# Kernel tuning notes

Hardware: AMD Instinct MI355X
Metric: run time of the kernel (lower is better)

## Reference

```python
import jax, jax.numpy as jnp
import numpy as np

N = 100000       # nodes
E = 1600000      # edges (avg degree 16)
D = 128          # features_dim = hidden_dim = out_dim
G = 3            # group_num
NUM = 50000      # nodes present in all time groups
ALPHA = 0.2      # LeakyReLU slope
W_SCALE = 0.05


def setup_inputs() -> dict:
    key = jax.random.key(0)
    ks = jax.random.split(key, 8)
    x = jax.random.normal(ks[0], (N, D), jnp.float32)
    edge_index = jax.random.randint(ks[1], (2, E), 0, N, dtype=jnp.int64)
    past = jax.random.normal(ks[2], (G - 1, NUM, D), jnp.float32)
    W1 = jax.random.normal(ks[3], (2 * D, D), jnp.float32) * W_SCALE
    W2 = jax.random.normal(ks[4], (2 * D, D), jnp.float32) * W_SCALE
    W0 = jax.random.normal(ks[5], (D, D), jnp.float32) * W_SCALE
    Wp = jax.random.normal(ks[6], (G - 1, D, D), jnp.float32) * W_SCALE
    W_T = jax.random.normal(ks[7], (2 * D, D), jnp.float32) * W_SCALE
    return {"x": x, "past": past, "W1": W1, "W2": W2, "W0": W0,
            "Wp": Wp, "W_T": W_T, "edge_index": edge_index, "num": NUM}


def reference(x, past, W1, W2, W0, Wp, W_T, edge_index, num):
    src, dst = edge_index[0], edge_index[1]
    n = x.shape[0]
    deg = jax.ops.segment_sum(jnp.ones(src.shape[0], x.dtype), dst, num_segments=n)
    deg = jnp.maximum(deg, 1.0)[:, None]

    def sage_layer(h, W):
        # mean-aggregate neighbors, concat with self, linear + ReLU
        agg = jax.ops.segment_sum(h[src], dst, num_segments=n) / deg
        return jax.nn.relu(jnp.concatenate([h, agg], axis=1) @ W)

    feat = sage_layer(x, W1)      # [N, D]
    feat = sage_layer(feat, W2)   # [N, D]

    # temporal mean aggregation (dropout is identity in eval mode)
    time_feat = (feat[:num] @ W0 + jnp.einsum('knd,kde->ne', past, Wp)) / G
    fused = jnp.concatenate([feat[:num], time_feat], axis=1) @ W_T  # [num, D]
    f = jax.nn.leaky_relu(fused, ALPHA)
    f = f / jnp.maximum(jnp.linalg.norm(f, axis=1, keepdims=True), 1e-12)
    return jnp.concatenate([f, feat[num:]], axis=0)  # [N, D]
```

## Files before the change

### kernel.cpp

```cpp
#include <hip/hip_runtime.h>

#define FD 128
#define CAP 64
#define BSH 9
#define BINSZ 512
#define NBMAX 256

typedef __attribute__((ext_vector_type(8))) short bf16x8;
typedef __attribute__((ext_vector_type(4))) float f32x4;

__device__ __forceinline__ float bflo(unsigned v) { return __uint_as_float(v << 16); }
__device__ __forceinline__ float bfhi(unsigned v) { return __uint_as_float(v & 0xffff0000u); }
__device__ __forceinline__ unsigned short f2b(float f) {
  unsigned u = __float_as_uint(f);
  return (unsigned short)((u + 0x7fffu + ((u >> 16) & 1u)) >> 16);
}
__device__ __forceinline__ unsigned pack2(float x, float y) {
  return (unsigned)f2b(x) | ((unsigned)f2b(y) << 16);
}

#if __has_builtin(__builtin_amdgcn_fdot2_f32_bf16)
#define HAVE_DOT2 1
typedef __attribute__((ext_vector_type(2))) __bf16 bf16x2;
__device__ __forceinline__ float dot2acc(unsigned v, unsigned w, float acc) {
  return __builtin_amdgcn_fdot2_f32_bf16(__builtin_bit_cast(bf16x2, v),
                                         __builtin_bit_cast(bf16x2, w), acc, false);
}
#endif

__device__ __forceinline__ void wpack_tile(const float* __restrict__ W,
                                           unsigned short* __restrict__ Wf,
                                           int nkt, int tt, int lane) {
  int ct = tt & 7, kt = tt >> 3;
  int m = lane & 15, q = lane >> 4;
  int nn = ct * 16 + m;
  int k0 = kt * 32 + q * 8;
  unsigned short tmp[8];
#pragma unroll
  for (int j = 0; j < 8; ++j) tmp[j] = f2b(W[(size_t)(k0 + j) * FD + nn]);
  unsigned short* dst = Wf + ((size_t)(ct * nkt + kt) * 64 + lane) * 8;
  *(uint4*)dst = *(uint4*)tmp;
}

__global__ __launch_bounds__(256) void k_prep(const float4* __restrict__ x4,
                                              unsigned short* __restrict__ xb, int total4,
                                              const int* __restrict__ dst,
                                              int* __restrict__ binCnt, int E, int n, int NB,
                                              const float* __restrict__ W1,
                                              const float* __restrict__ W2,
                                              const float* __restrict__ W0,
                                              const float* __restrict__ Wp,
                                              const float* __restrict__ WT,
                                              unsigned short* __restrict__ w1f,
                                              unsigned short* __restrict__ w2f,
                                              unsigned short* __restrict__ wcf,
                                              unsigned short* __restrict__ wtf,
                                              unsigned short* __restrict__ f1b,
                                              int XCB, int HB) {
  __shared__ int lh[NBMAX];
  int b = blockIdx.x, tid = threadIdx.x;

  if (b < XCB) {
    int i = b * 256 + tid;
    if (i < total4) {
      float4 v = x4[i];
      *(uint2*)&xb[(size_t)i * 4] = make_uint2(pack2(v.x, v.y), pack2(v.z, v.w));
    }
    return;
  }
  b -= XCB;
  if (b < HB) {
    for (int i = tid; i < NB; i += 256) lh[i] = 0;
    __syncthreads();
    for (int e = b * 256 + tid; e < E; e += HB * 256) {
      unsigned d = (unsigned)dst[e];
      if (d < (unsigned)n) atomicAdd(&lh[d >> BSH], 1);
    }
    __syncthreads();
    for (int i = tid; i < NB; i += 256) {
      int c = lh[i];
      if (c) atomicAdd(&binCnt[i], c);
    }
    return;
  }
  b -= HB;
  if (b < 72) {
    int t4 = b * 4 + (tid >> 6);
    int lane = tid & 63;
    if (t4 < 64) wpack_tile(W1, w1f, 8, t4, lane);
    else if (t4 < 128) wpack_tile(W2, w2f, 8, t4 - 64, lane);
    else if (t4 < 192) wpack_tile(WT, wtf, 8, t4 - 128, lane);
    else {
      int tt = t4 - 192;
      int ct = tt & 7, kt = tt >> 3;
      const float* src = kt < 4 ? W0 : (kt < 8 ? Wp : (Wp + FD * FD));
      int ktl = kt & 3;
      int m = lane & 15, q = lane >> 4;
      int nn = ct * 16 + m;
      int k0 = ktl * 32 + q * 8;
      unsigned short tmp[8];
#pragma unroll
      for (int j = 0; j < 8; ++j) tmp[j] = f2b(src[(size_t)(k0 + j) * FD + nn]);
      unsigned short* dstp = wcf + ((size_t)(ct * 12 + kt) * 64 + lane) * 8;
      *(uint4*)dstp = *(uint4*)tmp;
    }
    return;
  }
  if (tid < 64) ((unsigned*)&xb[(size_t)n * FD])[tid] = 0u;
  else if (tid < 128) ((unsigned*)&f1b[(size_t)n * FD])[tid - 64] = 0u;
}

__global__ __launch_bounds__(256) void k_binscatter(const int* __restrict__ src,
                                                    const int* __restrict__ dst,
                                                    const int* __restrict__ binCnt,
                                                    int* __restrict__ binCur,
                                                    unsigned* __restrict__ binned,
                                                    int E, int n, int NB) {
  __shared__ int sbuf[NBMAX], sstart[NBMAX], lcnt[NBMAX], lbase[NBMAX];
  int t = threadIdx.x;
  int v0 = (t < NB) ? binCnt[t] : 0;
  sbuf[t] = v0;
  __syncthreads();
  for (int off = 1; off < 256; off <<= 1) {
    int v = (t >= off) ? sbuf[t - off] : 0;
    __syncthreads();
    sbuf[t] += v;
    __syncthreads();
  }
  sstart[t] = sbuf[t] - v0;
  lcnt[t] = 0;
  __syncthreads();

  const int CH = 4096;
  int e0 = blockIdx.x * CH;
  int se[16], de[16];
#pragma unroll
  for (int k = 0; k < 16; ++k) {
    int e = e0 + k * 256 + t;
    int ok = e < E;
    unsigned s = ok ? (unsigned)src[e] : 0u;
    unsigned d = ok ? (unsigned)dst[e] : 0u;
    if (s >= (unsigned)n) s = 0;
    ok = ok && d < (unsigned)n;
    se[k] = (int)s;
    de[k] = ok ? (int)d : -1;
    if (ok) atomicAdd(&lcnt[d >> BSH], 1);
  }
  __syncthreads();
  for (int i = t; i < NB; i += 256) {
    int c = lcnt[i];
    lbase[i] = c ? (sstart[i] + atomicAdd(&binCur[i], c)) : 0;
    lcnt[i] = 0;
  }
  __syncthreads();
#pragma unroll
  for (int k = 0; k < 16; ++k) {
    if (de[k] >= 0) {
      int bb = de[k] >> BSH;
      int p = lbase[bb] + atomicAdd(&lcnt[bb], 1);
      binned[p] = ((unsigned)(de[k] & (BINSZ - 1)) << 23) | (unsigned)se[k];
    }
  }
}

__global__ __launch_bounds__(256) void k_bucket2(const unsigned* __restrict__ binned,
                                                 const int* __restrict__ binCnt,
                                                 int* __restrict__ cnt,
                                                 int* __restrict__ idx, int n, int NB) {
  __shared__ int sbuf[NBMAX];
  __shared__ int lcnt[BINSZ];
  int bin = blockIdx.x, t = threadIdx.x;
  int v0 = (t < NB) ? binCnt[t] : 0;
  sbuf[t] = v0;
  __syncthreads();
  for (int off = 1; off < 256; off <<= 1) {
    int v = (t >= off) ? sbuf[t - off] : 0;
    __syncthreads();
    sbuf[t] += v;
    __syncthreads();
  }
  int c0 = binCnt[bin];
  int s0 = sbuf[bin] - c0;
  lcnt[t] = 0;
  lcnt[t + 256] = 0;
  __syncthreads();

  int base = bin << BSH;
  for (int i = t; i < c0; i += 256) {
    unsigned pr = binned[s0 + i];
    int dlow = (int)(pr >> 23);
    int p = atomicAdd(&lcnt[dlow], 1);
    if (p < CAP) idx[(size_t)(base + dlow) * CAP + p] = (int)(pr & 0x7FFFFFu);
  }
  __syncthreads();
  for (int d0 = t; d0 < BINSZ; d0 += 256) {
    int d = base + d0;
    if (d < n) cnt[d] = lcnt[d0];
  }
}

__global__ __launch_bounds__(256) void k_sage(const unsigned* __restrict__ hb,
                                              const int* __restrict__ cnt,
                                              const int* __restrict__ idx,
                                              const unsigned short* __restrict__ Wf,
                                              float* __restrict__ outf,
                                              unsigned short* __restrict__ outb,
                                              int nbThr, int n) {
  __shared__ unsigned short sa[32][264];
  int tid = threadIdx.x;
  int lane = tid & 63, wv = tid >> 6;
  int rowBase = blockIdx.x * 32;

  for (int i = tid; i < 32 * 32; i += 256) {
    int r = i >> 5, cp = i & 31;
    int gr = rowBase + r;
    uint2 v = (gr < n) ? *(const uint2*)&hb[(size_t)gr * 64 + cp * 2] : make_uint2(0u, 0u);
    *(uint2*)&sa[r][cp * 4] = v;
  }

  int rbase = wv * 8;
  const int* ip = idx + (size_t)(rowBase + rbase) * CAP;
  int vidx[8];
  int c[8];
  int maxc = 0;
#pragma unroll
  for (int j = 0; j < 8; ++j) {
    int gr = rowBase + rbase + j;
    int cj = (gr < n) ? min(cnt[gr], CAP) : 0;
    cj = __builtin_amdgcn_readfirstlane(cj);
    c[j] = cj;
    maxc = max(maxc, cj);
    int v = 0;
    if (lane < cj) v = ip[j * CAP + lane];
    vidx[j] = v;
  }
  maxc = min(maxc, CAP);

#ifdef HAVE_DOT2
  float sxa[8], dxa[8];
#pragma unroll
  for (int j = 0; j < 8; ++j) { sxa[j] = 0.f; dxa[j] = 0.f; }
  const unsigned ONES = 0x3F803F80u;
  const unsigned PMON = 0xBF803F80u;

  for (int e = 0; e < maxc; e += 4) {
    int l1 = min(e + 1, CAP - 1), l2 = min(e + 2, CAP - 1), l3 = min(e + 3, CAP - 1);
    unsigned v[8][4];
#pragma unroll
    for (int j = 0; j < 8; ++j) {
      int s0 = __builtin_amdgcn_readlane(vidx[j], e);
      int s1 = __builtin_amdgcn_readlane(vidx[j], l1);
      int s2 = __builtin_amdgcn_readlane(vidx[j], l2);
      int s3 = __builtin_amdgcn_readlane(vidx[j], l3);
      s0 = (e     < c[j]) ? s0 : n;
      s1 = (e + 1 < c[j]) ? s1 : n;
      s2 = (e + 2 < c[j]) ? s2 : n;
      s3 = (e + 3 < c[j]) ? s3 : n;
      v[j][0] = hb[(size_t)s0 * 64 + lane];
      v[j][1] = hb[(size_t)s1 * 64 + lane];
      v[j][2] = hb[(size_t)s2 * 64 + lane];
      v[j][3] = hb[(size_t)s3 * 64 + lane];
    }
#pragma unroll
    for (int j = 0; j < 8; ++j) {
#pragma unroll
      for (int k = 0; k < 4; ++k) {
        sxa[j] = dot2acc(v[j][k], ONES, sxa[j]);
        dxa[j] = dot2acc(v[j][k], PMON, dxa[j]);
      }
    }
  }
#pragma unroll
  for (int j = 0; j < 8; ++j) {
    float inv = 0.5f / fmaxf((float)c[j], 1.0f);
    float ax = (sxa[j] + dxa[j]) * inv;
    float ay = (sxa[j] - dxa[j]) * inv;
    *(unsigned*)&sa[rbase + j][FD + lane * 2] = pack2(ax, ay);
  }
#else
  float ax[8], ay[8];
#pragma unroll
  for (int j = 0; j < 8; ++j) { ax[j] = 0.f; ay[j] = 0.f; }

  for (int e = 0; e < maxc; e += 4) {
    int l1 = min(e + 1, CAP - 1), l2 = min(e + 2, CAP - 1), l3 = min(e + 3, CAP - 1);
    unsigned v[8][4];
#pragma unroll
    for (int j = 0; j < 8; ++j) {
      int s0 = __builtin_amdgcn_readlane(vidx[j], e);
      int s1 = __builtin_amdgcn_readlane(vidx[j], l1);
      int s2 = __builtin_amdgcn_readlane(vidx[j], l2);
      int s3 = __builtin_amdgcn_readlane(vidx[j], l3);
      s0 = (e     < c[j]) ? s0 : n;
      s1 = (e + 1 < c[j]) ? s1 : n;
      s2 = (e + 2 < c[j]) ? s2 : n;
      s3 = (e + 3 < c[j]) ? s3 : n;
      v[j][0] = hb[(size_t)s0 * 64 + lane];
      v[j][1] = hb[(size_t)s1 * 64 + lane];
      v[j][2] = hb[(size_t)s2 * 64 + lane];
      v[j][3] = hb[(size_t)s3 * 64 + lane];
    }
#pragma unroll
    for (int j = 0; j < 8; ++j) {
#pragma unroll
      for (int k = 0; k < 4; ++k) {
        ax[j] += bflo(v[j][k]);
        ay[j] += bfhi(v[j][k]);
      }
    }
  }
#pragma unroll
  for (int j = 0; j < 8; ++j) {
    float inv = 1.0f / fmaxf((float)c[j], 1.0f);
    *(unsigned*)&sa[rbase + j][FD + lane * 2] = pack2(ax[j] * inv, ay[j] * inv);
  }
#endif
  __syncthreads();

  int m = lane & 15, q = lane >> 4;
  f32x4 z = {0.f, 0.f, 0.f, 0.f};
  f32x4 acc[2][2] = {{z, z}, {z, z}};
  int ct0 = wv * 2;
  const bf16x8* WfV = (const bf16x8*)Wf;
#pragma unroll
  for (int kt = 0; kt < 8; ++kt) {
    bf16x8 a0 = *(const bf16x8*)&sa[m][kt * 32 + q * 8];
    bf16x8 a1 = *(const bf16x8*)&sa[16 + m][kt * 32 + q * 8];
    bf16x8 b0 = WfV[(size_t)(ct0 * 8 + kt) * 64 + lane];
    bf16x8 b1 = WfV[(size_t)((ct0 + 1) * 8 + kt) * 64 + lane];
    acc[0][0] = __builtin_amdgcn_mfma_f32_16x16x32_bf16(a0, b0, acc[0][0], 0, 0, 0);
    acc[0][1] = __builtin_amdgcn_mfma_f32_16x16x32_bf16(a0, b1, acc[0][1], 0, 0, 0);
    acc[1][0] = __builtin_amdgcn_mfma_f32_16x16x32_bf16(a1, b0, acc[1][0], 0, 0, 0);
    acc[1][1] = __builtin_amdgcn_mfma_f32_16x16x32_bf16(a1, b1, acc[1][1], 0, 0, 0);
  }

#pragma unroll
  for (int rt = 0; rt < 2; ++rt) {
#pragma unroll
    for (int t = 0; t < 2; ++t) {
      int col = (ct0 + t) * 16 + m;
#pragma unroll
      for (int reg = 0; reg < 4; ++reg) {
        int gr = rowBase + rt * 16 + q * 4 + reg;
        if (gr < n) {
          float v = fmaxf(acc[rt][t][reg], 0.f);
          if (gr < nbThr)
            outb[(size_t)gr * FD + col] = f2b(v);
          else
            outf[(size_t)gr * FD + col] = v;
        }
      }
    }
  }
}

__global__ __launch_bounds__(256) void k_fuse(const unsigned short* __restrict__ feat2b,
                                              const float* __restrict__ past,
                                              const unsigned short* __restrict__ Wcf,
                                              const unsigned short* __restrict__ Wtf,
                                              float* __restrict__ out, int num) {
  __shared__ unsigned short sa[32][392];
  __shared__ float so[32][132];
  int tid = threadIdx.x;
  int lane = tid & 63, wv = tid >> 6;
  int base = blockIdx.x * 32;

  const unsigned* f2u = (const unsigned*)feat2b;
  for (int i = tid; i < 32 * 64; i += 256) {
    int r = i >> 6, cp = i & 63;
    int gr = base + r;
    unsigned uvf = 0u;
    float2 v0 = {0.f, 0.f}, v1 = {0.f, 0.f};
    if (gr < num) {
      uvf = f2u[(size_t)gr * 64 + cp];
      v0 = *(const float2*)&past[(size_t)gr * FD + cp * 2];
      v1 = *(const float2*)&past[(size_t)num * FD + (size_t)gr * FD + cp * 2];
    }
    *(unsigned*)&sa[r][cp * 2]       = uvf;
    *(unsigned*)&sa[r][FD + cp * 2]  = pack2(v0.x, v0.y);
    *(unsigned*)&sa[r][256 + cp * 2] = pack2(v1.x, v1.y);
  }
  __syncthreads();

  int m = lane & 15, q = lane >> 4;
  int ct0 = wv * 2;
  f32x4 z = {0.f, 0.f, 0.f, 0.f};
  const bf16x8* WcV = (const bf16x8*)Wcf;
  const bf16x8* WtV = (const bf16x8*)Wtf;

  f32x4 acc[2][2] = {{z, z}, {z, z}};
#pragma unroll
  for (int kt = 0; kt < 12; ++kt) {
    bf16x8 a0 = *(const bf16x8*)&sa[m][kt * 32 + q * 8];
    bf16x8 a1 = *(const bf16x8*)&sa[16 + m][kt * 32 + q * 8];
    bf16x8 b0 = WcV[(size_t)(ct0 * 12 + kt) * 64 + lane];
    bf16x8 b1 = WcV[(size_t)((ct0 + 1) * 12 + kt) * 64 + lane];
    acc[0][0] = __builtin_amdgcn_mfma_f32_16x16x32_bf16(a0, b0, acc[0][0], 0, 0, 0);
    acc[0][1] = __builtin_amdgcn_mfma_f32_16x16x32_bf16(a0, b1, acc[0][1], 0, 0, 0);
    acc[1][0] = __builtin_amdgcn_mfma_f32_16x16x32_bf16(a1, b0, acc[1][0], 0, 0, 0);
    acc[1][1] = __builtin_amdgcn_mfma_f32_16x16x32_bf16(a1, b1, acc[1][1], 0, 0, 0);
  }
  __syncthreads();

  const float inv3 = 1.0f / 3.0f;
#pragma unroll
  for (int rt = 0; rt < 2; ++rt)
#pragma unroll
    for (int t = 0; t < 2; ++t) {
      int col = (ct0 + t) * 16 + m;
#pragma unroll
      for (int reg = 0; reg < 4; ++reg)
        sa[rt * 16 + q * 4 + reg][FD + col] = f2b(acc[rt][t][reg] * inv3);
    }
  __syncthreads();

  f32x4 acc2[2][2] = {{z, z}, {z, z}};
#pragma unroll
  for (int kt = 0; kt < 8; ++kt) {
    bf16x8 a0 = *(const bf16x8*)&sa[m][kt * 32 + q * 8];
    bf16x8 a1 = *(const bf16x8*)&sa[16 + m][kt * 32 + q * 8];
    bf16x8 b0 = WtV[(size_t)(ct0 * 8 + kt) * 64 + lane];
    bf16x8 b1 = WtV[(size_t)((ct0 + 1) * 8 + kt) * 64 + lane];
    acc2[0][0] = __builtin_amdgcn_mfma_f32_16x16x32_bf16(a0, b0, acc2[0][0], 0, 0, 0);
    acc2[0][1] = __builtin_amdgcn_mfma_f32_16x16x32_bf16(a0, b1, acc2[0][1], 0, 0, 0);
    acc2[1][0] = __builtin_amdgcn_mfma_f32_16x16x32_bf16(a1, b0, acc2[1][0], 0, 0, 0);
    acc2[1][1] = __builtin_amdgcn_mfma_f32_16x16x32_bf16(a1, b1, acc2[1][1], 0, 0, 0);
  }

#pragma unroll
  for (int rt = 0; rt < 2; ++rt)
#pragma unroll
    for (int t = 0; t < 2; ++t) {
      int col = (ct0 + t) * 16 + m;
#pragma unroll
      for (int reg = 0; reg < 4; ++reg) {
        float v = acc2[rt][t][reg];
        so[rt * 16 + q * 4 + reg][col] = v > 0.f ? v : 0.2f * v;
      }
    }
  __syncthreads();

#pragma unroll
  for (int j = 0; j < 8; ++j) {
    int r = wv * 8 + j;
    float v0 = so[r][lane * 2], v1 = so[r][lane * 2 + 1];
    float ss = v0 * v0 + v1 * v1;
#pragma unroll
    for (int mk = 32; mk >= 1; mk >>= 1) ss += __shfl_xor(ss, mk, 64);
    float inv = 1.0f / fmaxf(sqrtf(ss), 1e-12f);
    int gr = base + r;
    if (gr < num) {
      float2 o = {v0 * inv, v1 * inv};
      *(float2*)&out[(size_t)gr * FD + lane * 2] = o;
    }
  }
}

extern "C" void kernel_launch(void* const* d_in, const int* in_sizes, int n_in,
                              void* d_out, int out_size, void* d_ws, size_t ws_size,
                              hipStream_t stream) {
  const float* x    = (const float*)d_in[0];
  const float* past = (const float*)d_in[1];
  const float* W1   = (const float*)d_in[2];
  const float* W2   = (const float*)d_in[3];
  const float* W0   = (const float*)d_in[4];
  const float* Wp   = (const float*)d_in[5];
  const float* WT   = (const float*)d_in[6];
  const int*   ei   = (const int*)d_in[7];

  int N   = in_sizes[0] / FD;
  int NUM = in_sizes[1] / (2 * FD);
  int E   = in_sizes[7] / 2;
  const int* src = ei;
  const int* dst = ei + E;
  float* out = (float*)d_out;

  int NB = (N + BINSZ - 1) >> BSH;

  char* p = (char*)d_ws;
  int* cnt      = (int*)p;  p += (((size_t)N * 4 + 255) & ~(size_t)255);
  int* idx      = (int*)p;  p += (size_t)N * CAP * 4;
  int* binCnt   = (int*)p;  p += NBMAX * 4;
  int* binCur   = (int*)p;  p += NBMAX * 4;
  unsigned* binned = (unsigned*)p; p += (size_t)E * 4;
  unsigned short* xb  = (unsigned short*)p; p += (size_t)(N + 1) * FD * 2;
  unsigned short* f1b = (unsigned short*)p; p += (size_t)(N + 1) * FD * 2;
  unsigned short* w1f = (unsigned short*)p; p += (size_t)8 * 8 * 64 * 8 * 2;
  unsigned short* w2f = (unsigned short*)p; p += (size_t)8 * 8 * 64 * 8 * 2;
  unsigned short* wcf = (unsigned short*)p; p += (size_t)8 * 12 * 64 * 8 * 2;
  unsigned short* wtf = (unsigned short*)p;
  unsigned short* f2b_buf = xb;

  hipMemsetAsync(binCnt, 0, 2 * NBMAX * sizeof(int), stream);

  int total4 = N * 32;
  int XCB = (total4 + 255) / 256;
  int HB  = 400;
  k_prep<<<XCB + HB + 72 + 1, 256, 0, stream>>>((const float4*)x, xb, total4,
                                                dst, binCnt, E, N, NB,
                                                W1, W2, W0, Wp, WT,
                                                w1f, w2f, wcf, wtf, f1b, XCB, HB);

  k_binscatter<<<(E + 4095) / 4096, 256, 0, stream>>>(src, dst, binCnt, binCur, binned, E, N, NB);
  k_bucket2<<<NB, 256, 0, stream>>>(binned, binCnt, cnt, idx, N, NB);

  int sageGrid = (N + 31) / 32;
  k_sage<<<sageGrid, 256, 0, stream>>>((const unsigned*)xb, cnt, idx, w1f, nullptr, f1b, N, N);
  k_sage<<<sageGrid, 256, 0, stream>>>((const unsigned*)f1b, cnt, idx, w2f, out, f2b_buf, NUM, N);
  k_fuse<<<(NUM + 31) / 32, 256, 0, stream>>>(f2b_buf, past, wcf, wtf, out, NUM);
}
```

Before: 388.2 us.

## Replace two-pass binned CSR build with direct global-atomic adjacency fill

Replaces the histogram, bin-scatter and per-bin bucketing passes with a single kernel. That kernel does one global atomicAdd per edge on the destination count and writes the source index straight into a fixed-capacity adjacency slot. The count array is now zeroed inside the prep kernel rather than by a memset. This drops two kernel launches and the intermediate binned edge buffer, but trades them for scattered global atomics and scattered writes into idx. Neighbor order within a slot also becomes nondeterministic.

```diff
diff --git a/kernel.cpp b/kernel.cpp
--- a/kernel.cpp
+++ b/kernel.cpp
@@ -2,9 +2,6 @@
 
 #define FD 128
 #define CAP 64
-#define BSH 9
-#define BINSZ 512
-#define NBMAX 256
 
 typedef __attribute__((ext_vector_type(8))) short bf16x8;
 typedef __attribute__((ext_vector_type(4))) float f32x4;
@@ -44,8 +41,7 @@
 
 __global__ __launch_bounds__(256) void k_prep(const float4* __restrict__ x4,
                                               unsigned short* __restrict__ xb, int total4,
-                                              const int* __restrict__ dst,
-                                              int* __restrict__ binCnt, int E, int n, int NB,
+                                              int* __restrict__ cnt, int cntInts,
                                               const float* __restrict__ W1,
                                               const float* __restrict__ W2,
                                               const float* __restrict__ W0,
@@ -56,8 +52,7 @@
                                               unsigned short* __restrict__ wcf,
                                               unsigned short* __restrict__ wtf,
                                               unsigned short* __restrict__ f1b,
-                                              int XCB, int HB) {
-  __shared__ int lh[NBMAX];
+                                              int n, int XCB, int CZB) {
   int b = blockIdx.x, tid = threadIdx.x;
 
   if (b < XCB) {
@@ -69,21 +64,12 @@
     return;
   }
   b -= XCB;
-  if (b < HB) {
-    for (int i = tid; i < NB; i += 256) lh[i] = 0;
-    __syncthreads();
-    for (int e = b * 256 + tid; e < E; e += HB * 256) {
-      unsigned d = (unsigned)dst[e];
-      if (d < (unsigned)n) atomicAdd(&lh[d >> BSH], 1);
-    }
-    __syncthreads();
-    for (int i = tid; i < NB; i += 256) {
-      int c = lh[i];
-      if (c) atomicAdd(&binCnt[i], c);
-    }
+  if (b < CZB) {
+    int i4 = (b * 256 + tid) * 4;
+    if (i4 < cntInts) *(uint4*)&cnt[i4] = make_uint4(0u, 0u, 0u, 0u);
     return;
   }
-  b -= HB;
+  b -= CZB;
   if (b < 72) {
     int t4 = b * 4 + (tid >> 6);
     int lane = tid & 63;
@@ -110,92 +96,17 @@
   else if (tid < 128) ((unsigned*)&f1b[(size_t)n * FD])[tid - 64] = 0u;
 }
 
-__global__ __launch_bounds__(256) void k_binscatter(const int* __restrict__ src,
-                                                    const int* __restrict__ dst,
-                                                    const int* __restrict__ binCnt,
-                                                    int* __restrict__ binCur,
-                                                    unsigned* __restrict__ binned,
-                                                    int E, int n, int NB) {
-  __shared__ int sbuf[NBMAX], sstart[NBMAX], lcnt[NBMAX], lbase[NBMAX];
-  int t = threadIdx.x;
-  int v0 = (t < NB) ? binCnt[t] : 0;
-  sbuf[t] = v0;
-  __syncthreads();
-  for (int off = 1; off < 256; off <<= 1) {
-    int v = (t >= off) ? sbuf[t - off] : 0;
-    __syncthreads();
-    sbuf[t] += v;
-    __syncthreads();
-  }
-  sstart[t] = sbuf[t] - v0;
-  lcnt[t] = 0;
-  __syncthreads();
-
-  const int CH = 4096;
-  int e0 = blockIdx.x * CH;
-  int se[16], de[16];
-#pragma unroll
-  for (int k = 0; k < 16; ++k) {
-    int e = e0 + k * 256 + t;
-    int ok = e < E;
-    unsigned s = ok ? (unsigned)src[e] : 0u;
-    unsigned d = ok ? (unsigned)dst[e] : 0u;
-    if (s >= (unsigned)n) s = 0;
-    ok = ok && d < (unsigned)n;
-    se[k] = (int)s;
-    de[k] = ok ? (int)d : -1;
-    if (ok) atomicAdd(&lcnt[d >> BSH], 1);
-  }
-  __syncthreads();
-  for (int i = t; i < NB; i += 256) {
-    int c = lcnt[i];
-    lbase[i] = c ? (sstart[i] + atomicAdd(&binCur[i], c)) : 0;
-    lcnt[i] = 0;
-  }
-  __syncthreads();
-#pragma unroll
-  for (int k = 0; k < 16; ++k) {
-    if (de[k] >= 0) {
-      int bb = de[k] >> BSH;
-      int p = lbase[bb] + atomicAdd(&lcnt[bb], 1);
-      binned[p] = ((unsigned)(de[k] & (BINSZ - 1)) << 23) | (unsigned)se[k];
-    }
-  }
-}
-
-__global__ __launch_bounds__(256) void k_bucket2(const unsigned* __restrict__ binned,
-                                                 const int* __restrict__ binCnt,
-                                                 int* __restrict__ cnt,
-                                                 int* __restrict__ idx, int n, int NB) {
-  __shared__ int sbuf[NBMAX];
-  __shared__ int lcnt[BINSZ];
-  int bin = blockIdx.x, t = threadIdx.x;
-  int v0 = (t < NB) ? binCnt[t] : 0;
-  sbuf[t] = v0;
-  __syncthreads();
-  for (int off = 1; off < 256; off <<= 1) {
-    int v = (t >= off) ? sbuf[t - off] : 0;
-    __syncthreads();
-    sbuf[t] += v;
-    __syncthreads();
-  }
-  int c0 = binCnt[bin];
-  int s0 = sbuf[bin] - c0;
-  lcnt[t] = 0;
-  lcnt[t + 256] = 0;
-  __syncthreads();
-
-  int base = bin << BSH;
-  for (int i = t; i < c0; i += 256) {
-    unsigned pr = binned[s0 + i];
-    int dlow = (int)(pr >> 23);
-    int p = atomicAdd(&lcnt[dlow], 1);
-    if (p < CAP) idx[(size_t)(base + dlow) * CAP + p] = (int)(pr & 0x7FFFFFu);
-  }
-  __syncthreads();
-  for (int d0 = t; d0 < BINSZ; d0 += 256) {
-    int d = base + d0;
-    if (d < n) cnt[d] = lcnt[d0];
+__global__ __launch_bounds__(256) void k_build(const int* __restrict__ src,
+                                               const int* __restrict__ dst,
+                                               int* __restrict__ cnt,
+                                               int* __restrict__ idx, int E, int n) {
+  int e = blockIdx.x * 256 + threadIdx.x;
+  if (e >= E) return;
+  unsigned s = (unsigned)src[e], d = (unsigned)dst[e];
+  if (s >= (unsigned)n) s = 0;
+  if (d < (unsigned)n) {
+    int p = atomicAdd(&cnt[d], 1);
+    if (p < CAP) idx[(size_t)d * CAP + p] = (int)s;
   }
 }
 
@@ -475,14 +386,11 @@
   const int* dst = ei + E;
   float* out = (float*)d_out;
 
-  int NB = (N + BINSZ - 1) >> BSH;
-
   char* p = (char*)d_ws;
-  int* cnt      = (int*)p;  p += (((size_t)N * 4 + 255) & ~(size_t)255);
+  size_t cntBytes = ((size_t)N * 4 + 255) & ~(size_t)255;
+  int cntInts = (int)(cntBytes / 4);
+  int* cnt      = (int*)p;  p += cntBytes;
   int* idx      = (int*)p;  p += (size_t)N * CAP * 4;
-  int* binCnt   = (int*)p;  p += NBMAX * 4;
-  int* binCur   = (int*)p;  p += NBMAX * 4;
-  unsigned* binned = (unsigned*)p; p += (size_t)E * 4;
   unsigned short* xb  = (unsigned short*)p; p += (size_t)(N + 1) * FD * 2;
   unsigned short* f1b = (unsigned short*)p; p += (size_t)(N + 1) * FD * 2;
   unsigned short* w1f = (unsigned short*)p; p += (size_t)8 * 8 * 64 * 8 * 2;
@@ -491,18 +399,15 @@
   unsigned short* wtf = (unsigned short*)p;
   unsigned short* f2b_buf = xb;
 
-  hipMemsetAsync(binCnt, 0, 2 * NBMAX * sizeof(int), stream);
-
   int total4 = N * 32;
   int XCB = (total4 + 255) / 256;
-  int HB  = 400;
-  k_prep<<<XCB + HB + 72 + 1, 256, 0, stream>>>((const float4*)x, xb, total4,
-                                                dst, binCnt, E, N, NB,
-                                                W1, W2, W0, Wp, WT,
-                                                w1f, w2f, wcf, wtf, f1b, XCB, HB);
-
-  k_binscatter<<<(E + 4095) / 4096, 256, 0, stream>>>(src, dst, binCnt, binCur, binned, E, N, NB);
-  k_bucket2<<<NB, 256, 0, stream>>>(binned, binCnt, cnt, idx, N, NB);
+  int CZB = (cntInts / 4 + 255) / 256;
+  k_prep<<<XCB + CZB + 72 + 1, 256, 0, stream>>>((const float4*)x, xb, total4,
+                                                 cnt, cntInts,
+                                                 W1, W2, W0, Wp, WT,
+                                                 w1f, w2f, wcf, wtf, f1b, N, XCB, CZB);
+
+  k_build<<<(E + 255) / 256, 256, 0, stream>>>(src, dst, cnt, idx, E, N);
 
   int sageGrid = (N + 31) / 32;
   k_sage<<<sageGrid, 256, 0, stream>>>((const unsigned*)xb, cnt, idx, w1f, nullptr, f1b, N, N);
```

Result: slower. 437.4 us (+12.7%).

## Fuse temporal fusion kernel into second SAGE layer epilogue

Applied to the files above, without the earlier changes.

The second SAGE layer is templated so that, for row blocks below num, its ReLU output stays in shared memory as bf16 and the temporal projection, W_T matmul, LeakyReLU and L2 normalization run in the same block. This removes the bf16 feat2 write and re-read through global memory and one kernel launch. In exchange the fused kernel uses a larger shared-memory tile, which may lower occupancy during the latency-bound gather phase. Blocks with rows at or beyond num write fp32 output directly and exit early.

```diff
diff --git a/kernel.cpp b/kernel.cpp
--- a/kernel.cpp
+++ b/kernel.cpp
@@ -199,14 +199,19 @@
   }
 }
 
+template <int FUSE>
 __global__ __launch_bounds__(256) void k_sage(const unsigned* __restrict__ hb,
                                               const int* __restrict__ cnt,
                                               const int* __restrict__ idx,
                                               const unsigned short* __restrict__ Wf,
+                                              const float* __restrict__ past,
+                                              const unsigned short* __restrict__ wcf,
+                                              const unsigned short* __restrict__ wtf,
                                               float* __restrict__ outf,
                                               unsigned short* __restrict__ outb,
-                                              int nbThr, int n) {
-  __shared__ unsigned short sa[32][264];
+                                              int n, int num) {
+  constexpr int SAW = FUSE ? 392 : 264;
+  __shared__ unsigned short sa[32][SAW];
   int tid = threadIdx.x;
   int lane = tid & 63, wv = tid >> 6;
   int rowBase = blockIdx.x * 32;
@@ -281,7 +286,6 @@
   float ax[8], ay[8];
 #pragma unroll
   for (int j = 0; j < 8; ++j) { ax[j] = 0.f; ay[j] = 0.f; }
-
   for (int e = 0; e < maxc; e += 4) {
     int l1 = min(e + 1, CAP - 1), l2 = min(e + 2, CAP - 1), l3 = min(e + 3, CAP - 1);
     unsigned v[8][4];
@@ -334,71 +338,83 @@
     acc[1][1] = __builtin_amdgcn_mfma_f32_16x16x32_bf16(a1, b1, acc[1][1], 0, 0, 0);
   }
 
-#pragma unroll
-  for (int rt = 0; rt < 2; ++rt) {
+  if (!FUSE) {
+#pragma unroll
+    for (int rt = 0; rt < 2; ++rt)
+#pragma unroll
+      for (int t = 0; t < 2; ++t) {
+        int col = (ct0 + t) * 16 + m;
+#pragma unroll
+        for (int reg = 0; reg < 4; ++reg) {
+          int gr = rowBase + rt * 16 + q * 4 + reg;
+          if (gr < n) outb[(size_t)gr * FD + col] = f2b(fmaxf(acc[rt][t][reg], 0.f));
+        }
+      }
+    return;
+  }
+
+  if (rowBase >= num) {
+#pragma unroll
+    for (int rt = 0; rt < 2; ++rt)
+#pragma unroll
+      for (int t = 0; t < 2; ++t) {
+        int col = (ct0 + t) * 16 + m;
+#pragma unroll
+        for (int reg = 0; reg < 4; ++reg) {
+          int gr = rowBase + rt * 16 + q * 4 + reg;
+          if (gr < n) outf[(size_t)gr * FD + col] = fmaxf(acc[rt][t][reg], 0.f);
+        }
+      }
+    return;
+  }
+
+  __syncthreads();
+
+#pragma unroll
+  for (int rt = 0; rt < 2; ++rt)
 #pragma unroll
     for (int t = 0; t < 2; ++t) {
       int col = (ct0 + t) * 16 + m;
 #pragma unroll
       for (int reg = 0; reg < 4; ++reg) {
-        int gr = rowBase + rt * 16 + q * 4 + reg;
-        if (gr < n) {
-          float v = fmaxf(acc[rt][t][reg], 0.f);
-          if (gr < nbThr)
-            outb[(size_t)gr * FD + col] = f2b(v);
-          else
-            outf[(size_t)gr * FD + col] = v;
+        int r = rt * 16 + q * 4 + reg;
+        int gr = rowBase + r;
+        float v = fmaxf(acc[rt][t][reg], 0.f);
+        if (gr >= num) {
+          if (gr < n) outf[(size_t)gr * FD + col] = v;
+          v = 0.f;
         }
+        sa[r][col] = f2b(v);
       }
     }
-  }
-}
-
-__global__ __launch_bounds__(256) void k_fuse(const unsigned short* __restrict__ feat2b,
-                                              const float* __restrict__ past,
-                                              const unsigned short* __restrict__ Wcf,
-                                              const unsigned short* __restrict__ Wtf,
-                                              float* __restrict__ out, int num) {
-  __shared__ unsigned short sa[32][392];
-  __shared__ float so[32][132];
-  int tid = threadIdx.x;
-  int lane = tid & 63, wv = tid >> 6;
-  int base = blockIdx.x * 32;
-
-  const unsigned* f2u = (const unsigned*)feat2b;
+
   for (int i = tid; i < 32 * 64; i += 256) {
     int r = i >> 6, cp = i & 63;
-    int gr = base + r;
-    unsigned uvf = 0u;
+    int gr = rowBase + r;
     float2 v0 = {0.f, 0.f}, v1 = {0.f, 0.f};
     if (gr < num) {
-      uvf = f2u[(size_t)gr * 64 + cp];
       v0 = *(const float2*)&past[(size_t)gr * FD + cp * 2];
       v1 = *(const float2*)&past[(size_t)num * FD + (size_t)gr * FD + cp * 2];
     }
-    *(unsigned*)&sa[r][cp * 2]       = uvf;
     *(unsigned*)&sa[r][FD + cp * 2]  = pack2(v0.x, v0.y);
     *(unsigned*)&sa[r][256 + cp * 2] = pack2(v1.x, v1.y);
   }
   __syncthreads();
 
-  int m = lane & 15, q = lane >> 4;
-  int ct0 = wv * 2;
-  f32x4 z = {0.f, 0.f, 0.f, 0.f};
-  const bf16x8* WcV = (const bf16x8*)Wcf;
-  const bf16x8* WtV = (const bf16x8*)Wtf;
-
-  f32x4 acc[2][2] = {{z, z}, {z, z}};
+  const bf16x8* WcV = (const bf16x8*)wcf;
+  const bf16x8* WtV = (const bf16x8*)wtf;
+
+  f32x4 accA[2][2] = {{z, z}, {z, z}};
 #pragma unroll
   for (int kt = 0; kt < 12; ++kt) {
     bf16x8 a0 = *(const bf16x8*)&sa[m][kt * 32 + q * 8];
     bf16x8 a1 = *(const bf16x8*)&sa[16 + m][kt * 32 + q * 8];
     bf16x8 b0 = WcV[(size_t)(ct0 * 12 + kt) * 64 + lane];
     bf16x8 b1 = WcV[(size_t)((ct0 + 1) * 12 + kt) * 64 + lane];
-    acc[0][0] = __builtin_amdgcn_mfma_f32_16x16x32_bf16(a0, b0, acc[0][0], 0, 0, 0);
-    acc[0][1] = __builtin_amdgcn_mfma_f32_16x16x32_bf16(a0, b1, acc[0][1], 0, 0, 0);
-    acc[1][0] = __builtin_amdgcn_mfma_f32_16x16x32_bf16(a1, b0, acc[1][0], 0, 0, 0);
-    acc[1][1] = __builtin_amdgcn_mfma_f32_16x16x32_bf16(a1, b1, acc[1][1], 0, 0, 0);
+    accA[0][0] = __builtin_amdgcn_mfma_f32_16x16x32_bf16(a0, b0, accA[0][0], 0, 0, 0);
+    accA[0][1] = __builtin_amdgcn_mfma_f32_16x16x32_bf16(a0, b1, accA[0][1], 0, 0, 0);
+    accA[1][0] = __builtin_amdgcn_mfma_f32_16x16x32_bf16(a1, b0, accA[1][0], 0, 0, 0);
+    accA[1][1] = __builtin_amdgcn_mfma_f32_16x16x32_bf16(a1, b1, accA[1][1], 0, 0, 0);
   }
   __syncthreads();
 
@@ -410,7 +426,7 @@
       int col = (ct0 + t) * 16 + m;
 #pragma unroll
       for (int reg = 0; reg < 4; ++reg)
-        sa[rt * 16 + q * 4 + reg][FD + col] = f2b(acc[rt][t][reg] * inv3);
+        sa[rt * 16 + q * 4 + reg][FD + col] = f2b(accA[rt][t][reg] * inv3);
     }
   __syncthreads();
 
@@ -426,7 +442,9 @@
     acc2[1][0] = __builtin_amdgcn_mfma_f32_16x16x32_bf16(a1, b0, acc2[1][0], 0, 0, 0);
     acc2[1][1] = __builtin_amdgcn_mfma_f32_16x16x32_bf16(a1, b1, acc2[1][1], 0, 0, 0);
   }
-
+  __syncthreads();
+
+  float* sof = (float*)&sa[0][0];
 #pragma unroll
   for (int rt = 0; rt < 2; ++rt)
 #pragma unroll
@@ -435,7 +453,7 @@
 #pragma unroll
       for (int reg = 0; reg < 4; ++reg) {
         float v = acc2[rt][t][reg];
-        so[rt * 16 + q * 4 + reg][col] = v > 0.f ? v : 0.2f * v;
+        sof[(rt * 16 + q * 4 + reg) * 132 + col] = v > 0.f ? v : 0.2f * v;
       }
     }
   __syncthreads();
@@ -443,15 +461,15 @@
 #pragma unroll
   for (int j = 0; j < 8; ++j) {
     int r = wv * 8 + j;
-    float v0 = so[r][lane * 2], v1 = so[r][lane * 2 + 1];
+    float v0 = sof[r * 132 + lane * 2], v1 = sof[r * 132 + lane * 2 + 1];
     float ss = v0 * v0 + v1 * v1;
 #pragma unroll
     for (int mk = 32; mk >= 1; mk >>= 1) ss += __shfl_xor(ss, mk, 64);
     float inv = 1.0f / fmaxf(sqrtf(ss), 1e-12f);
-    int gr = base + r;
+    int gr = rowBase + r;
     if (gr < num) {
       float2 o = {v0 * inv, v1 * inv};
-      *(float2*)&out[(size_t)gr * FD + lane * 2] = o;
+      *(float2*)&outf[(size_t)gr * FD + lane * 2] = o;
     }
   }
 }
@@ -489,7 +507,6 @@
   unsigned short* w2f = (unsigned short*)p; p += (size_t)8 * 8 * 64 * 8 * 2;
   unsigned short* wcf = (unsigned short*)p; p += (size_t)8 * 12 * 64 * 8 * 2;
   unsigned short* wtf = (unsigned short*)p;
-  unsigned short* f2b_buf = xb;
 
   hipMemsetAsync(binCnt, 0, 2 * NBMAX * sizeof(int), stream);
 
@@ -505,7 +522,10 @@
   k_bucket2<<<NB, 256, 0, stream>>>(binned, binCnt, cnt, idx, N, NB);
 
   int sageGrid = (N + 31) / 32;
-  k_sage<<<sageGrid, 256, 0, stream>>>((const unsigned*)xb, cnt, idx, w1f, nullptr, f1b, N, N);
-  k_sage<<<sageGrid, 256, 0, stream>>>((const unsigned*)f1b, cnt, idx, w2f, out, f2b_buf, NUM, N);
-  k_fuse<<<(NUM + 31) / 32, 256, 0, stream>>>(f2b_buf, past, wcf, wtf, out, NUM);
-}
+  k_sage<0><<<sageGrid, 256, 0, stream>>>((const unsigned*)xb, cnt, idx, w1f,
+                                          nullptr, nullptr, nullptr,
+                                          nullptr, f1b, N, N);
+  k_sage<1><<<sageGrid, 256, 0, stream>>>((const unsigned*)f1b, cnt, idx, w2f,
+                                          past, wcf, wtf,
+                                          out, nullptr, N, NUM);
+}
```

After: 370.7 us. 4.5% less time.
